# Kernel optimization log

Hardware: AMD Instinct MI355X
Metric: run time of the kernel (lower is better)

## Reference

```python
import jax, jax.numpy as jnp
import numpy as np

ROUTING_ITERATIONS = 3


def squash(x):
    # squared norm over the capsule output dim
    sq = jnp.sum(x * x, axis=-1, keepdims=True)
    scale = sq / (1.0 + sq)
    return scale * x / jnp.sqrt(sq)


def setup_inputs() -> dict:
    key = jax.random.key(0)
    k1, k2 = jax.random.split(key)
    B, N, IN_C, K, OUT_C = 256, 1152, 8, 10, 16
    u = jax.random.normal(k1, (B, N, IN_C), dtype=jnp.float32)
    W = jax.random.normal(k2, (K, N, IN_C, OUT_C), dtype=jnp.float32)
    return {"u": u, "W": W}


def reference(u, W):
    # u: [B, N, in_c]; W: [K, N, in_c, out_c]
    # torch: u_hat = matmul(u[None,:,:,None,:], W[:,None]) -> [K, B, N, 1, out_c]
    u_hat = jnp.einsum('bni,knio->kbno', u, W)  # [K, B, N, out_c]
    b_ij = jnp.zeros_like(u_hat)
    v_j = None
    for it in range(ROUTING_ITERATIONS):
        c_ij = jax.nn.softmax(b_ij, axis=2)               # softmax over N, per out_c channel
        s_j = jnp.sum(c_ij * u_hat, axis=2, keepdims=True)  # [K, B, 1, out_c]
        v_j = squash(s_j)
        if it < ROUTING_ITERATIONS - 1:
            a_ij = jnp.sum(u_hat * v_j, axis=-1, keepdims=True)  # [K, B, N, 1]
            b_ij = b_ij + a_ij
    # match torch output shape [K, B, 1, 1, out_c]
    return v_j[:, :, :, None, :]
```

## Files before the change

kernel.cpp:

```cpp
#include <hip/hip_runtime.h>
#include <hip/hip_fp16.h>

#define Bsz 256
#define Nn  1152
#define Kk  10
#define NT  576
#define NW  9
#define SJ  1154

#define W_ELEMS (Kk*Nn*128)
#define U_ELEMS (Bsz*Nn*8)

__device__ __forceinline__ unsigned pkh2(float x, float y) {
    __half2 h = __floats2half2_rn(x, y);
    return *reinterpret_cast<unsigned*>(&h);
}
__device__ __forceinline__ float2 uph2(unsigned v) {
    __half2 h;
    *reinterpret_cast<unsigned*>(&h) = v;
    return __half22float2(h);
}
__device__ __forceinline__ void up8(const uint4 q, float f[8]) {
    float2 a = uph2(q.x), b = uph2(q.y), c = uph2(q.z), d = uph2(q.w);
    f[0]=a.x; f[1]=a.y; f[2]=b.x; f[3]=b.y; f[4]=c.x; f[5]=c.y; f[6]=d.x; f[7]=d.y;
}

__global__ void cvt_kernel(const float* __restrict__ W, const float* __restrict__ u,
                           __half2* __restrict__ Wh, __half2* __restrict__ uh) {
    const int idx = blockIdx.x * blockDim.x + threadIdx.x;
    const int wg = W_ELEMS / 8;
    const float4* p;
    __half2* o;
    if (idx < wg) {
        p = (const float4*)W + (size_t)idx * 2;
        o = Wh + (size_t)idx * 4;
    } else {
        const int j = idx - wg;
        p = (const float4*)u + (size_t)j * 2;
        o = uh + (size_t)j * 4;
    }
    const float4 a = p[0], b = p[1];
    o[0] = __floats2half2_rn(a.x, a.y);
    o[1] = __floats2half2_rn(a.z, a.w);
    o[2] = __floats2half2_rn(b.x, b.y);
    o[3] = __floats2half2_rn(b.z, b.w);
}

template<bool HALF>
__global__ __launch_bounds__(NT, 2)
void digitcaps_kernel(const float* __restrict__ u32, const float* __restrict__ W32,
                      const __half* __restrict__ uh, const __half* __restrict__ Wh,
                      float* __restrict__ out)
{
    const int t    = threadIdx.x;
    const int lane = t & 63;
    const int wav  = t >> 6;
    const int bg   = blockIdx.x;
    const int k    = blockIdx.y;
    const int b0   = bg * 2;

    __shared__ uint2    uhS[8 * SJ];
    __shared__ unsigned cS2[Nn];
    __shared__ float    redS[2 * NW * 17];
    __shared__ __align__(16) float vS[32];
    __shared__ float    mS[2];

    {
        const int oh   = t & 1;
        const int nsub = t >> 1;
        for (int r = 0; r < 4; ++r) {
            const int n = r * 288 + nsub;
            float ua[8], ub[8];
            if (HALF) {
                const uint4 qa = *(const uint4*)(uh + ((size_t)b0 * Nn + n) * 8);
                const uint4 qb = *(const uint4*)(uh + ((size_t)(b0 + 1) * Nn + n) * 8);
                up8(qa, ua); up8(qb, ub);
            } else {
                const float4* up0 = (const float4*)(u32 + ((size_t)b0 * Nn + n) * 8);
                const float4* up1 = (const float4*)(u32 + ((size_t)(b0 + 1) * Nn + n) * 8);
                const float4 x0 = up0[0], x1 = up0[1];
                const float4 y0 = up1[0], y1 = up1[1];
                ua[0]=x0.x; ua[1]=x0.y; ua[2]=x0.z; ua[3]=x0.w;
                ua[4]=x1.x; ua[5]=x1.y; ua[6]=x1.z; ua[7]=x1.w;
                ub[0]=y0.x; ub[1]=y0.y; ub[2]=y0.z; ub[3]=y0.w;
                ub[4]=y1.x; ub[5]=y1.y; ub[6]=y1.z; ub[7]=y1.w;
            }
            float a0[8], a1[8];
            #pragma unroll
            for (int o = 0; o < 8; ++o) { a0[o] = 0.f; a1[o] = 0.f; }
            #pragma unroll
            for (int i = 0; i < 8; ++i) {
                float wv[8];
                if (HALF) {
                    const uint4 qw = *(const uint4*)(Wh + ((size_t)(k * Nn + n)) * 128 + i * 16 + oh * 8);
                    up8(qw, wv);
                } else {
                    const float4* wp = (const float4*)(W32 + ((size_t)k * Nn + n) * 128) + oh * 2 + i * 4;
                    const float4 w0 = wp[0], w1 = wp[1];
                    wv[0]=w0.x; wv[1]=w0.y; wv[2]=w0.z; wv[3]=w0.w;
                    wv[4]=w1.x; wv[5]=w1.y; wv[6]=w1.z; wv[7]=w1.w;
                }
                const float x = ua[i], y = ub[i];
                #pragma unroll
                for (int o = 0; o < 8; ++o) { a0[o] += x * wv[o]; a1[o] += y * wv[o]; }
            }
            #pragma unroll
            for (int jj = 0; jj < 4; ++jj) {
                const int j = oh * 4 + jj;
                uhS[j * SJ + n] = make_uint2(pkh2(a0[2*jj], a0[2*jj+1]),
                                             pkh2(a1[2*jj], a1[2*jj+1]));
            }
        }
    }
    __syncthreads();

    float lg0[2] = {0.f, 0.f}, lg1[2] = {0.f, 0.f};
    float v0[16], v1[16];
    const int j_s = lane & 7;
    const int g_s = lane >> 3;

    for (int it = 0; it < 3; ++it) {
        if (it > 0) {
            #pragma unroll
            for (int r = 0; r < 2; ++r) {
                const int n = t + r * NT;
                float acc0 = 0.f, acc1 = 0.f;
                #pragma unroll
                for (int j = 0; j < 8; ++j) {
                    const uint2 q = uhS[j * SJ + n];
                    const float2 f0 = uph2(q.x);
                    const float2 f1 = uph2(q.y);
                    acc0 += f0.x * v0[2*j] + f0.y * v0[2*j+1];
                    acc1 += f1.x * v1[2*j] + f1.y * v1[2*j+1];
                }
                lg0[r] += acc0;
                lg1[r] += acc1;
            }
            float m0 = fmaxf(lg0[0], lg0[1]);
            float m1 = fmaxf(lg1[0], lg1[1]);
            #pragma unroll
            for (int off = 1; off <= 32; off <<= 1) {
                m0 = fmaxf(m0, __shfl_xor(m0, off));
                m1 = fmaxf(m1, __shfl_xor(m1, off));
            }
            if (lane == 0) { redS[wav] = m0; redS[NW + wav] = m1; }
            __syncthreads();
            if (t < 2) {
                float m = redS[t * NW];
                for (int w = 1; w < NW; ++w) m = fmaxf(m, redS[t * NW + w]);
                mS[t] = m;
            }
            __syncthreads();
            m0 = mS[0]; m1 = mS[1];
            const float e00 = __expf(lg0[0] - m0), e01 = __expf(lg0[1] - m0);
            const float e10 = __expf(lg1[0] - m1), e11 = __expf(lg1[1] - m1);
            cS2[t]      = pkh2(e00, e10);
            cS2[t + NT] = pkh2(e01, e11);
            __syncthreads();
        }

        float2 sp0 = {0.f, 0.f}, sp1 = {0.f, 0.f};
        float dp0 = 0.f, dp1 = 0.f;
        #pragma unroll
        for (int cc = 0; cc < 16; ++cc) {
            const int n = cc * 72 + wav * 8 + g_s;
            float c0, c1;
            if (it == 0) { c0 = 1.f; c1 = 1.f; }
            else { const float2 c2 = uph2(cS2[n]); c0 = c2.x; c1 = c2.y; }
            const uint2 q = uhS[j_s * SJ + n];
            const float2 f0 = uph2(q.x);
            const float2 f1 = uph2(q.y);
            sp0.x += c0 * f0.x; sp0.y += c0 * f0.y;
            sp1.x += c1 * f1.x; sp1.y += c1 * f1.y;
            dp0 += c0; dp1 += c1;
        }
        #pragma unroll
        for (int off = 8; off <= 32; off <<= 1) {
            sp0.x += __shfl_xor(sp0.x, off);
            sp0.y += __shfl_xor(sp0.y, off);
            sp1.x += __shfl_xor(sp1.x, off);
            sp1.y += __shfl_xor(sp1.y, off);
            dp0   += __shfl_xor(dp0,   off);
            dp1   += __shfl_xor(dp1,   off);
        }
        if (lane < 8) {
            redS[(0*NW + wav)*17 + 2*j_s    ] = sp0.x;
            redS[(0*NW + wav)*17 + 2*j_s + 1] = sp0.y;
            redS[(1*NW + wav)*17 + 2*j_s    ] = sp1.x;
            redS[(1*NW + wav)*17 + 2*j_s + 1] = sp1.y;
        }
        if (lane == 0) {
            redS[(0*NW + wav)*17 + 16] = dp0;
            redS[(1*NW + wav)*17 + 16] = dp1;
        }
        __syncthreads();

        if (t < 32) {
            const int b = t >> 4, o = t & 15;
            float s = 0.f, d = 0.f;
            #pragma unroll
            for (int w = 0; w < NW; ++w) {
                s += redS[(b*NW + w)*17 + o];
                d += redS[(b*NW + w)*17 + 16];
            }
            s /= d;
            float s2 = s * s;
            #pragma unroll
            for (int off = 1; off <= 8; off <<= 1) s2 += __shfl_xor(s2, off);
            const float scale = (s2 / (1.f + s2)) * rsqrtf(fmaxf(s2, 1e-30f));
            const float v = s * scale;
            vS[b*16 + o] = v;
            if (it == 2) out[((size_t)k * Bsz + b0 + b) * 16 + o] = v;
        }
        if (it == 2) break;
        __syncthreads();

        {
            const float4* vp = (const float4*)vS;
            #pragma unroll
            for (int q4 = 0; q4 < 4; ++q4) {
                *(float4*)&v0[4*q4] = vp[q4];
                *(float4*)&v1[4*q4] = vp[4 + q4];
            }
        }
    }
}

extern "C" void kernel_launch(void* const* d_in, const int* in_sizes, int n_in,
                              void* d_out, int out_size, void* d_ws, size_t ws_size,
                              hipStream_t stream) {
    const float* u = (const float*)d_in[0];
    const float* W = (const float*)d_in[1];
    float* out = (float*)d_out;
    const size_t need = (size_t)(W_ELEMS + U_ELEMS) * sizeof(__half);
    if (ws_size >= need) {
        __half* Wh = (__half*)d_ws;
        __half* uh = (__half*)((char*)d_ws + (size_t)W_ELEMS * sizeof(__half));
        cvt_kernel<<<dim3((W_ELEMS + U_ELEMS) / 8 / 256), dim3(256), 0, stream>>>(
            W, u, (__half2*)Wh, (__half2*)uh);
        digitcaps_kernel<true><<<dim3(128, 10), dim3(NT), 0, stream>>>(
            nullptr, nullptr, uh, Wh, out);
    } else {
        digitcaps_kernel<false><<<dim3(128, 10), dim3(NT), 0, stream>>>(
            u, W, nullptr, nullptr, out);
    }
}
```

Baseline: 130.2 us.

## Use packed fp16 dot2 instructions and transpose W layout for dot-product access

The fp16 conversion kernel now transposes W through shared memory, so each output channel's 8 input weights sit contiguously as packed half2 values. The u_hat computation, the agreement logits and the weighted sums then use v_fdot2 (packed fp16 dot with fp32 accumulate) instead of unpacking to fp32 and doing scalar FMAs. In the weighted-sum loop, pairs of n are merged with byte permutes so each dot2 covers two capsules, and v is kept as packed halves. This cuts ALU work and conversion overhead, at the cost of the extra shared-memory transpose in the convert step and reduced precision from rounding v and the coefficients to fp16.

```diff
diff --git a/kernel.cpp b/kernel.cpp
--- a/kernel.cpp
+++ b/kernel.cpp
@@ -10,40 +10,64 @@
 
 #define W_ELEMS (Kk*Nn*128)
 #define U_ELEMS (Bsz*Nn*8)
-
-__device__ __forceinline__ unsigned pkh2(float x, float y) {
+#define WCELLS  (Kk*Nn)
+#define WBLKS   (WCELLS/16)
+#define UBLKS   (U_ELEMS/8/256)
+
+typedef _Float16 hf2_t __attribute__((ext_vector_type(2)));
+
+static __device__ __forceinline__ unsigned pkh2(float x, float y) {
     __half2 h = __floats2half2_rn(x, y);
     return *reinterpret_cast<unsigned*>(&h);
 }
-__device__ __forceinline__ float2 uph2(unsigned v) {
+static __device__ __forceinline__ float2 uph2(unsigned v) {
     __half2 h;
     *reinterpret_cast<unsigned*>(&h) = v;
     return __half22float2(h);
 }
-__device__ __forceinline__ void up8(const uint4 q, float f[8]) {
-    float2 a = uph2(q.x), b = uph2(q.y), c = uph2(q.z), d = uph2(q.w);
-    f[0]=a.x; f[1]=a.y; f[2]=b.x; f[3]=b.y; f[4]=c.x; f[5]=c.y; f[6]=d.x; f[7]=d.y;
-}
+static __device__ __forceinline__ float fdot2u(unsigned a, unsigned b, float c) {
+    union { unsigned u; hf2_t h; } A, B;
+    A.u = a; B.u = b;
+    return __builtin_amdgcn_fdot2(A.h, B.h, c, false);
+}
+
+#define PERM_LO 0x01000504u
+#define PERM_HI 0x03020706u
+#define ONE2    0x3C003C00u
 
 __global__ void cvt_kernel(const float* __restrict__ W, const float* __restrict__ u,
-                           __half2* __restrict__ Wh, __half2* __restrict__ uh) {
-    const int idx = blockIdx.x * blockDim.x + threadIdx.x;
-    const int wg = W_ELEMS / 8;
-    const float4* p;
-    __half2* o;
-    if (idx < wg) {
-        p = (const float4*)W + (size_t)idx * 2;
-        o = Wh + (size_t)idx * 4;
+                           unsigned* __restrict__ Wh, __half2* __restrict__ uh) {
+    const int t = threadIdx.x;
+    if ((int)blockIdx.x < WBLKS) {
+        __shared__ float ws[16 * 132];
+        const size_t base = (size_t)blockIdx.x * (16 * 128);
+        const float4* p = (const float4*)(W + base) + t * 2;
+        const float4 x = p[0], y = p[1];
+        {
+            const int e = t * 8;
+            float* d = ws + (e >> 7) * 132 + (e & 127);
+            d[0]=x.x; d[1]=x.y; d[2]=x.z; d[3]=x.w;
+            d[4]=y.x; d[5]=y.y; d[6]=y.z; d[7]=y.w;
+        }
+        __syncthreads();
+        const int c = t >> 4, o = t & 15;
+        const float* s = ws + c * 132 + o;
+        uint4 r;
+        r.x = pkh2(s[0*16], s[1*16]);
+        r.y = pkh2(s[2*16], s[3*16]);
+        r.z = pkh2(s[4*16], s[5*16]);
+        r.w = pkh2(s[6*16], s[7*16]);
+        *(uint4*)(Wh + ((size_t)blockIdx.x * 16 + c) * 64 + o * 4) = r;
     } else {
-        const int j = idx - wg;
-        p = (const float4*)u + (size_t)j * 2;
-        o = uh + (size_t)j * 4;
-    }
-    const float4 a = p[0], b = p[1];
-    o[0] = __floats2half2_rn(a.x, a.y);
-    o[1] = __floats2half2_rn(a.z, a.w);
-    o[2] = __floats2half2_rn(b.x, b.y);
-    o[3] = __floats2half2_rn(b.z, b.w);
+        const int j = ((int)blockIdx.x - WBLKS) * 256 + t;
+        const float4* p = (const float4*)u + (size_t)j * 2;
+        __half2* o = uh + (size_t)j * 4;
+        const float4 a = p[0], b = p[1];
+        o[0] = __floats2half2_rn(a.x, a.y);
+        o[1] = __floats2half2_rn(a.z, a.w);
+        o[2] = __floats2half2_rn(b.x, b.y);
+        o[3] = __floats2half2_rn(b.z, b.w);
+    }
 }
 
 template<bool HALF>
@@ -70,12 +94,22 @@
         const int nsub = t >> 1;
         for (int r = 0; r < 4; ++r) {
             const int n = r * 288 + nsub;
-            float ua[8], ub[8];
+            float a0[8], a1[8];
             if (HALF) {
                 const uint4 qa = *(const uint4*)(uh + ((size_t)b0 * Nn + n) * 8);
                 const uint4 qb = *(const uint4*)(uh + ((size_t)(b0 + 1) * Nn + n) * 8);
-                up8(qa, ua); up8(qb, ub);
+                #pragma unroll
+                for (int o = 0; o < 8; ++o) {
+                    const uint4 w = *(const uint4*)(Wh + (((size_t)(k * Nn + n)) * 16 + oh * 8 + o) * 8);
+                    float s0 = 0.f, s1 = 0.f;
+                    s0 = fdot2u(qa.x, w.x, s0); s1 = fdot2u(qb.x, w.x, s1);
+                    s0 = fdot2u(qa.y, w.y, s0); s1 = fdot2u(qb.y, w.y, s1);
+                    s0 = fdot2u(qa.z, w.z, s0); s1 = fdot2u(qb.z, w.z, s1);
+                    s0 = fdot2u(qa.w, w.w, s0); s1 = fdot2u(qb.w, w.w, s1);
+                    a0[o] = s0; a1[o] = s1;
+                }
             } else {
+                float ua[8], ub[8];
                 const float4* up0 = (const float4*)(u32 + ((size_t)b0 * Nn + n) * 8);
                 const float4* up1 = (const float4*)(u32 + ((size_t)(b0 + 1) * Nn + n) * 8);
                 const float4 x0 = up0[0], x1 = up0[1];
@@ -84,25 +118,19 @@
                 ua[4]=x1.x; ua[5]=x1.y; ua[6]=x1.z; ua[7]=x1.w;
                 ub[0]=y0.x; ub[1]=y0.y; ub[2]=y0.z; ub[3]=y0.w;
                 ub[4]=y1.x; ub[5]=y1.y; ub[6]=y1.z; ub[7]=y1.w;
-            }
-            float a0[8], a1[8];
-            #pragma unroll
-            for (int o = 0; o < 8; ++o) { a0[o] = 0.f; a1[o] = 0.f; }
-            #pragma unroll
-            for (int i = 0; i < 8; ++i) {
-                float wv[8];
-                if (HALF) {
-                    const uint4 qw = *(const uint4*)(Wh + ((size_t)(k * Nn + n)) * 128 + i * 16 + oh * 8);
-                    up8(qw, wv);
-                } else {
+                #pragma unroll
+                for (int o = 0; o < 8; ++o) { a0[o] = 0.f; a1[o] = 0.f; }
+                #pragma unroll
+                for (int i = 0; i < 8; ++i) {
                     const float4* wp = (const float4*)(W32 + ((size_t)k * Nn + n) * 128) + oh * 2 + i * 4;
                     const float4 w0 = wp[0], w1 = wp[1];
+                    float wv[8];
                     wv[0]=w0.x; wv[1]=w0.y; wv[2]=w0.z; wv[3]=w0.w;
                     wv[4]=w1.x; wv[5]=w1.y; wv[6]=w1.z; wv[7]=w1.w;
+                    const float x = ua[i], y = ub[i];
+                    #pragma unroll
+                    for (int o = 0; o < 8; ++o) { a0[o] += x * wv[o]; a1[o] += y * wv[o]; }
                 }
-                const float x = ua[i], y = ub[i];
-                #pragma unroll
-                for (int o = 0; o < 8; ++o) { a0[o] += x * wv[o]; a1[o] += y * wv[o]; }
             }
             #pragma unroll
             for (int jj = 0; jj < 4; ++jj) {
@@ -115,7 +143,7 @@
     __syncthreads();
 
     float lg0[2] = {0.f, 0.f}, lg1[2] = {0.f, 0.f};
-    float v0[16], v1[16];
+    unsigned vh0[8], vh1[8];
     const int j_s = lane & 7;
     const int g_s = lane >> 3;
 
@@ -128,10 +156,8 @@
                 #pragma unroll
                 for (int j = 0; j < 8; ++j) {
                     const uint2 q = uhS[j * SJ + n];
-                    const float2 f0 = uph2(q.x);
-                    const float2 f1 = uph2(q.y);
-                    acc0 += f0.x * v0[2*j] + f0.y * v0[2*j+1];
-                    acc1 += f1.x * v1[2*j] + f1.y * v1[2*j+1];
+                    acc0 = fdot2u(q.x, vh0[j], acc0);
+                    acc1 = fdot2u(q.y, vh1[j], acc1);
                 }
                 lg0[r] += acc0;
                 lg1[r] += acc1;
@@ -162,18 +188,31 @@
         float2 sp0 = {0.f, 0.f}, sp1 = {0.f, 0.f};
         float dp0 = 0.f, dp1 = 0.f;
         #pragma unroll
-        for (int cc = 0; cc < 16; ++cc) {
-            const int n = cc * 72 + wav * 8 + g_s;
-            float c0, c1;
-            if (it == 0) { c0 = 1.f; c1 = 1.f; }
-            else { const float2 c2 = uph2(cS2[n]); c0 = c2.x; c1 = c2.y; }
-            const uint2 q = uhS[j_s * SJ + n];
-            const float2 f0 = uph2(q.x);
-            const float2 f1 = uph2(q.y);
-            sp0.x += c0 * f0.x; sp0.y += c0 * f0.y;
-            sp1.x += c1 * f1.x; sp1.y += c1 * f1.y;
-            dp0 += c0; dp1 += c1;
-        }
+        for (int cc2 = 0; cc2 < 8; ++cc2) {
+            const int n0 = cc2 * 144 + wav * 8 + g_s;
+            const int n1 = n0 + 72;
+            const uint2 q0 = uhS[j_s * SJ + n0];
+            const uint2 q1 = uhS[j_s * SJ + n1];
+            unsigned cp0, cp1;
+            if (it == 0) { cp0 = ONE2; cp1 = ONE2; }
+            else {
+                const unsigned e0 = cS2[n0], e1 = cS2[n1];
+                cp0 = __builtin_amdgcn_perm(e0, e1, PERM_LO);
+                cp1 = __builtin_amdgcn_perm(e0, e1, PERM_HI);
+                dp0 = fdot2u(cp0, ONE2, dp0);
+                dp1 = fdot2u(cp1, ONE2, dp1);
+            }
+            const unsigned px0 = __builtin_amdgcn_perm(q0.x, q1.x, PERM_LO);
+            const unsigned py0 = __builtin_amdgcn_perm(q0.x, q1.x, PERM_HI);
+            const unsigned px1 = __builtin_amdgcn_perm(q0.y, q1.y, PERM_LO);
+            const unsigned py1 = __builtin_amdgcn_perm(q0.y, q1.y, PERM_HI);
+            sp0.x = fdot2u(px0, cp0, sp0.x);
+            sp0.y = fdot2u(py0, cp0, sp0.y);
+            sp1.x = fdot2u(px1, cp1, sp1.x);
+            sp1.y = fdot2u(py1, cp1, sp1.y);
+        }
+        if (it == 0) { dp0 = 16.f; dp1 = 16.f; }
+
         #pragma unroll
         for (int off = 8; off <= 32; off <<= 1) {
             sp0.x += __shfl_xor(sp0.x, off);
@@ -219,8 +258,11 @@
             const float4* vp = (const float4*)vS;
             #pragma unroll
             for (int q4 = 0; q4 < 4; ++q4) {
-                *(float4*)&v0[4*q4] = vp[q4];
-                *(float4*)&v1[4*q4] = vp[4 + q4];
+                const float4 a = vp[q4], b = vp[4 + q4];
+                vh0[2*q4]   = pkh2(a.x, a.y);
+                vh0[2*q4+1] = pkh2(a.z, a.w);
+                vh1[2*q4]   = pkh2(b.x, b.y);
+                vh1[2*q4+1] = pkh2(b.z, b.w);
             }
         }
     }
@@ -236,8 +278,8 @@
     if (ws_size >= need) {
         __half* Wh = (__half*)d_ws;
         __half* uh = (__half*)((char*)d_ws + (size_t)W_ELEMS * sizeof(__half));
-        cvt_kernel<<<dim3((W_ELEMS + U_ELEMS) / 8 / 256), dim3(256), 0, stream>>>(
-            W, u, (__half2*)Wh, (__half2*)uh);
+        cvt_kernel<<<dim3(WBLKS + UBLKS), dim3(256), 0, stream>>>(
+            W, u, (unsigned*)Wh, (__half2*)uh);
         digitcaps_kernel<true><<<dim3(128, 10), dim3(NT), 0, stream>>>(
             nullptr, nullptr, uh, Wh, out);
     } else {
```

After: 146.0 us. 1.12x slower.

## Process one batch element per block with smaller blocks and higher occupancy

Applied to the files above, without the earlier changes.

Each block now handles a single batch element instead of two, with 384 threads (6 waves) and a 6-blocks-per-CU launch bound, doubling the grid to 256x10. Shared memory per block roughly halves, so more blocks can be resident and more work is exposed for parallelism. In exchange, every W tile is now loaded once per batch element rather than shared across two, doubling W traffic from global memory/L2 during the u_hat computation.

```diff
diff --git a/kernel.cpp b/kernel.cpp
--- a/kernel.cpp
+++ b/kernel.cpp
@@ -4,23 +4,23 @@
 #define Bsz 256
 #define Nn  1152
 #define Kk  10
-#define NT  576
-#define NW  9
-#define SJ  1154
+#define NT  384
+#define NW  6
+#define S4  1160
 
 #define W_ELEMS (Kk*Nn*128)
 #define U_ELEMS (Bsz*Nn*8)
 
-__device__ __forceinline__ unsigned pkh2(float x, float y) {
+static __device__ __forceinline__ unsigned pkh2(float x, float y) {
     __half2 h = __floats2half2_rn(x, y);
     return *reinterpret_cast<unsigned*>(&h);
 }
-__device__ __forceinline__ float2 uph2(unsigned v) {
+static __device__ __forceinline__ float2 uph2(unsigned v) {
     __half2 h;
     *reinterpret_cast<unsigned*>(&h) = v;
     return __half22float2(h);
 }
-__device__ __forceinline__ void up8(const uint4 q, float f[8]) {
+static __device__ __forceinline__ void up8(const uint4 q, float f[8]) {
     float2 a = uph2(q.x), b = uph2(q.y), c = uph2(q.z), d = uph2(q.w);
     f[0]=a.x; f[1]=a.y; f[2]=b.x; f[3]=b.y; f[4]=c.x; f[5]=c.y; f[6]=d.x; f[7]=d.y;
 }
@@ -47,7 +47,7 @@
 }
 
 template<bool HALF>
-__global__ __launch_bounds__(NT, 2)
+__global__ __launch_bounds__(NT, 6)
 void digitcaps_kernel(const float* __restrict__ u32, const float* __restrict__ W32,
                       const __half* __restrict__ uh, const __half* __restrict__ Wh,
                       float* __restrict__ out)
@@ -55,39 +55,33 @@
     const int t    = threadIdx.x;
     const int lane = t & 63;
     const int wav  = t >> 6;
-    const int bg   = blockIdx.x;
+    const int b    = blockIdx.x;
     const int k    = blockIdx.y;
-    const int b0   = bg * 2;
-
-    __shared__ uint2    uhS[8 * SJ];
-    __shared__ unsigned cS2[Nn];
-    __shared__ float    redS[2 * NW * 17];
-    __shared__ __align__(16) float vS[32];
-    __shared__ float    mS[2];
+
+    __shared__ unsigned       uhS[8 * S4];
+    __shared__ unsigned short cS[Nn];
+    __shared__ float          redS[NW * 17];
+    __shared__ __align__(16) float vS[16];
+    __shared__ float          mS[1];
 
     {
         const int oh   = t & 1;
         const int nsub = t >> 1;
-        for (int r = 0; r < 4; ++r) {
-            const int n = r * 288 + nsub;
-            float ua[8], ub[8];
+        for (int r = 0; r < 6; ++r) {
+            const int n = r * 192 + nsub;
+            float ua[8];
             if (HALF) {
-                const uint4 qa = *(const uint4*)(uh + ((size_t)b0 * Nn + n) * 8);
-                const uint4 qb = *(const uint4*)(uh + ((size_t)(b0 + 1) * Nn + n) * 8);
-                up8(qa, ua); up8(qb, ub);
+                const uint4 qa = *(const uint4*)(uh + ((size_t)b * Nn + n) * 8);
+                up8(qa, ua);
             } else {
-                const float4* up0 = (const float4*)(u32 + ((size_t)b0 * Nn + n) * 8);
-                const float4* up1 = (const float4*)(u32 + ((size_t)(b0 + 1) * Nn + n) * 8);
+                const float4* up0 = (const float4*)(u32 + ((size_t)b * Nn + n) * 8);
                 const float4 x0 = up0[0], x1 = up0[1];
-                const float4 y0 = up1[0], y1 = up1[1];
                 ua[0]=x0.x; ua[1]=x0.y; ua[2]=x0.z; ua[3]=x0.w;
                 ua[4]=x1.x; ua[5]=x1.y; ua[6]=x1.z; ua[7]=x1.w;
-                ub[0]=y0.x; ub[1]=y0.y; ub[2]=y0.z; ub[3]=y0.w;
-                ub[4]=y1.x; ub[5]=y1.y; ub[6]=y1.z; ub[7]=y1.w;
-            }
-            float a0[8], a1[8];
-            #pragma unroll
-            for (int o = 0; o < 8; ++o) { a0[o] = 0.f; a1[o] = 0.f; }
+            }
+            float a0[8];
+            #pragma unroll
+            for (int o = 0; o < 8; ++o) a0[o] = 0.f;
             #pragma unroll
             for (int i = 0; i < 8; ++i) {
                 float wv[8];
@@ -100,108 +94,93 @@
                     wv[0]=w0.x; wv[1]=w0.y; wv[2]=w0.z; wv[3]=w0.w;
                     wv[4]=w1.x; wv[5]=w1.y; wv[6]=w1.z; wv[7]=w1.w;
                 }
-                const float x = ua[i], y = ub[i];
+                const float x = ua[i];
                 #pragma unroll
-                for (int o = 0; o < 8; ++o) { a0[o] += x * wv[o]; a1[o] += y * wv[o]; }
-            }
-            #pragma unroll
-            for (int jj = 0; jj < 4; ++jj) {
-                const int j = oh * 4 + jj;
-                uhS[j * SJ + n] = make_uint2(pkh2(a0[2*jj], a0[2*jj+1]),
-                                             pkh2(a1[2*jj], a1[2*jj+1]));
-            }
+                for (int o = 0; o < 8; ++o) a0[o] += x * wv[o];
+            }
+            #pragma unroll
+            for (int jj = 0; jj < 4; ++jj)
+                uhS[(oh * 4 + jj) * S4 + n] = pkh2(a0[2*jj], a0[2*jj+1]);
         }
     }
     __syncthreads();
 
-    float lg0[2] = {0.f, 0.f}, lg1[2] = {0.f, 0.f};
-    float v0[16], v1[16];
+    float lg[3] = {0.f, 0.f, 0.f};
+    float vv[16];
     const int j_s = lane & 7;
     const int g_s = lane >> 3;
 
     for (int it = 0; it < 3; ++it) {
         if (it > 0) {
             #pragma unroll
-            for (int r = 0; r < 2; ++r) {
+            for (int r = 0; r < 3; ++r) {
                 const int n = t + r * NT;
-                float acc0 = 0.f, acc1 = 0.f;
+                float acc = 0.f;
                 #pragma unroll
                 for (int j = 0; j < 8; ++j) {
-                    const uint2 q = uhS[j * SJ + n];
-                    const float2 f0 = uph2(q.x);
-                    const float2 f1 = uph2(q.y);
-                    acc0 += f0.x * v0[2*j] + f0.y * v0[2*j+1];
-                    acc1 += f1.x * v1[2*j] + f1.y * v1[2*j+1];
+                    const float2 f = uph2(uhS[j * S4 + n]);
+                    acc += f.x * vv[2*j] + f.y * vv[2*j+1];
                 }
-                lg0[r] += acc0;
-                lg1[r] += acc1;
-            }
-            float m0 = fmaxf(lg0[0], lg0[1]);
-            float m1 = fmaxf(lg1[0], lg1[1]);
-            #pragma unroll
-            for (int off = 1; off <= 32; off <<= 1) {
-                m0 = fmaxf(m0, __shfl_xor(m0, off));
-                m1 = fmaxf(m1, __shfl_xor(m1, off));
-            }
-            if (lane == 0) { redS[wav] = m0; redS[NW + wav] = m1; }
+                lg[r] += acc;
+            }
+            float m = fmaxf(fmaxf(lg[0], lg[1]), lg[2]);
+            #pragma unroll
+            for (int off = 1; off <= 32; off <<= 1)
+                m = fmaxf(m, __shfl_xor(m, off));
+            if (lane == 0) redS[wav] = m;
             __syncthreads();
-            if (t < 2) {
-                float m = redS[t * NW];
-                for (int w = 1; w < NW; ++w) m = fmaxf(m, redS[t * NW + w]);
-                mS[t] = m;
+            if (t == 0) {
+                float mm = redS[0];
+                #pragma unroll
+                for (int w = 1; w < NW; ++w) mm = fmaxf(mm, redS[w]);
+                mS[0] = mm;
             }
             __syncthreads();
-            m0 = mS[0]; m1 = mS[1];
-            const float e00 = __expf(lg0[0] - m0), e01 = __expf(lg0[1] - m0);
-            const float e10 = __expf(lg1[0] - m1), e11 = __expf(lg1[1] - m1);
-            cS2[t]      = pkh2(e00, e10);
-            cS2[t + NT] = pkh2(e01, e11);
+            m = mS[0];
+            #pragma unroll
+            for (int r = 0; r < 3; ++r) {
+                const __half eh = __float2half(__expf(lg[r] - m));
+                cS[t + r * NT] = *reinterpret_cast<const unsigned short*>(&eh);
+            }
             __syncthreads();
         }
 
-        float2 sp0 = {0.f, 0.f}, sp1 = {0.f, 0.f};
-        float dp0 = 0.f, dp1 = 0.f;
+        float2 sp = {0.f, 0.f};
+        float dp = 0.f;
         #pragma unroll
-        for (int cc = 0; cc < 16; ++cc) {
-            const int n = cc * 72 + wav * 8 + g_s;
-            float c0, c1;
-            if (it == 0) { c0 = 1.f; c1 = 1.f; }
-            else { const float2 c2 = uph2(cS2[n]); c0 = c2.x; c1 = c2.y; }
-            const uint2 q = uhS[j_s * SJ + n];
-            const float2 f0 = uph2(q.x);
-            const float2 f1 = uph2(q.y);
-            sp0.x += c0 * f0.x; sp0.y += c0 * f0.y;
-            sp1.x += c1 * f1.x; sp1.y += c1 * f1.y;
-            dp0 += c0; dp1 += c1;
+        for (int cc = 0; cc < 24; ++cc) {
+            const int n = cc * 48 + wav * 8 + g_s;
+            float c;
+            if (it == 0) c = 1.f;
+            else {
+                const unsigned short eb = cS[n];
+                c = __half2float(*reinterpret_cast<const __half*>(&eb));
+            }
+            const float2 f = uph2(uhS[j_s * S4 + n]);
+            sp.x += c * f.x;
+            sp.y += c * f.y;
+            dp   += c;
         }
         #pragma unroll
         for (int off = 8; off <= 32; off <<= 1) {
-            sp0.x += __shfl_xor(sp0.x, off);
-            sp0.y += __shfl_xor(sp0.y, off);
-            sp1.x += __shfl_xor(sp1.x, off);
-            sp1.y += __shfl_xor(sp1.y, off);
-            dp0   += __shfl_xor(dp0,   off);
-            dp1   += __shfl_xor(dp1,   off);
+            sp.x += __shfl_xor(sp.x, off);
+            sp.y += __shfl_xor(sp.y, off);
+            dp   += __shfl_xor(dp,   off);
         }
         if (lane < 8) {
-            redS[(0*NW + wav)*17 + 2*j_s    ] = sp0.x;
-            redS[(0*NW + wav)*17 + 2*j_s + 1] = sp0.y;
-            redS[(1*NW + wav)*17 + 2*j_s    ] = sp1.x;
-            redS[(1*NW + wav)*17 + 2*j_s + 1] = sp1.y;
-        }
-        if (lane == 0) {
-            redS[(0*NW + wav)*17 + 16] = dp0;
-            redS[(1*NW + wav)*17 + 16] = dp1;
-        }
+            redS[wav * 17 + 2*j_s    ] = sp.x;
+            redS[wav * 17 + 2*j_s + 1] = sp.y;
+        }
+        if (lane == 0) redS[wav * 17 + 16] = dp;
         __syncthreads();
 
-        if (t < 32) {
-            const int b = t >> 4, o = t & 15;
+        if (t < 16) {
+            const int o = t;
             float s = 0.f, d = 0.f;
             #pragma unroll
             for (int w = 0; w < NW; ++w) {
-                s += redS[(b*NW + w)*17 + o];
-                d += redS[(b*NW + w)*17 + 16];
+                s += redS[w * 17 + o];
+                d += redS[w * 17 + 16];
             }
             s /= d;
             float s2 = s * s;
@@ -209,8 +188,8 @@
             for (int off = 1; off <= 8; off <<= 1) s2 += __shfl_xor(s2, off);
             const float scale = (s2 / (1.f + s2)) * rsqrtf(fmaxf(s2, 1e-30f));
             const float v = s * scale;
-            vS[b*16 + o] = v;
-            if (it == 2) out[((size_t)k * Bsz + b0 + b) * 16 + o] = v;
+            vS[o] = v;
+            if (it == 2) out[((size_t)k * Bsz + b) * 16 + o] = v;
         }
         if (it == 2) break;
         __syncthreads();
@@ -218,10 +197,8 @@
         {
             const float4* vp = (const float4*)vS;
             #pragma unroll
-            for (int q4 = 0; q4 < 4; ++q4) {
-                *(float4*)&v0[4*q4] = vp[q4];
-                *(float4*)&v1[4*q4] = vp[4 + q4];
-            }
+            for (int q4 = 0; q4 < 4; ++q4)
+                *(float4*)&vv[4*q4] = vp[q4];
         }
     }
 }
@@ -238,10 +215,10 @@
         __half* uh = (__half*)((char*)d_ws + (size_t)W_ELEMS * sizeof(__half));
         cvt_kernel<<<dim3((W_ELEMS + U_ELEMS) / 8 / 256), dim3(256), 0, stream>>>(
             W, u, (__half2*)Wh, (__half2*)uh);
-        digitcaps_kernel<true><<<dim3(128, 10), dim3(NT), 0, stream>>>(
+        digitcaps_kernel<true><<<dim3(256, 10), dim3(NT), 0, stream>>>(
             nullptr, nullptr, uh, Wh, out);
     } else {
-        digitcaps_kernel<false><<<dim3(128, 10), dim3(NT), 0, stream>>>(
+        digitcaps_kernel<false><<<dim3(256, 10), dim3(NT), 0, stream>>>(
             u, W, nullptr, nullptr, out);
     }
 }
```

Result: no change. 128.5 us (-1.3%).
